# Performance work log

Measured on AMD Instinct MI355X. Metric: run time of the kernel, lower is better.

Reference implementation:

```python
import math
import jax, jax.numpy as jnp
import numpy as np

PH, PW = 16, 16
MAPPER_X = [0, 0, 6, 0, 0, 1, 1, 4, 5, 1, 3, 0, 0, 0, 3, 2]
MAPPER_Y = [0, 1, 0, 5, 2, 0, 2, 0, 0, 6, 0, 4, 6, 3, 5, 2]


def _make_dct_bases(ph, pw, mapper_x, mapper_y):
    bases = []
    for u, v in zip(mapper_x, mapper_y):
        Bu = np.cos(np.pi * (np.arange(ph) + 0.5) * u / ph) / math.sqrt(ph)
        if u != 0:
            Bu = Bu * math.sqrt(2)
        Bv = np.cos(np.pi * (np.arange(pw) + 0.5) * v / pw) / math.sqrt(pw)
        if v != 0:
            Bv = Bv * math.sqrt(2)
        bases.append(np.outer(Bu, Bv))
    return jnp.asarray(np.stack(bases, axis=0), dtype=jnp.float32)  # [M, ph, pw]


def setup_inputs() -> dict:
    key = jax.random.key(0)
    x = jax.random.normal(key, (16, 64, 224, 224), dtype=jnp.float32)
    dct_bases = _make_dct_bases(PH, PW, MAPPER_X, MAPPER_Y)
    return {"x": x, "dct_bases": dct_bases}


def reference(x, dct_bases):
    # x: [B, C, H, W]; dct_bases: [M, ph, pw]
    B, C, H, W = x.shape
    M, ph, pw = dct_bases.shape
    # H, W chosen divisible by ph, pw -> pad_h = pad_w = 0 (faithful to the no-pad path)
    Hp, Wp = H // ph, W // pw
    x_mean = x.mean(axis=1)                              # [B, H, W]
    patches = x_mean.reshape(B, Hp, ph, Wp, pw)          # non-overlapping unfold
    coeff = jnp.einsum('bhiwj,mij->bmhw', patches, dct_bases)  # [B, M, Hp, Wp]
    # nearest upsample by (ph, pw): broadcast each coeff over its patch footprint
    freq = jnp.broadcast_to(coeff[:, :, :, None, :, None], (B, M, Hp, ph, Wp, pw))
    return freq.reshape(B, M, H, W)
```

## Files before the change

### kernel.cpp

```cpp
#include <hip/hip_runtime.h>

#define B_   16
#define C_   64
#define H_   224
#define W_   224
#define M_   16
#define PH   16
#define PW   16
#define HP   14
#define WP   14
#define PLANE  (H_ * W_)
#define PLANE4 (PLANE / 4)
#define W4     (W_ / 4)
#define NSPLIT 2
#define CW     (W_ / NSPLIT)
#define CW4    (CW / 4)
#define WPB    (WP / NSPLIT)
#define SLOTS  (PH * CW4)
#define LSTW   116

typedef float f4 __attribute__((ext_vector_type(4)));

__global__ __launch_bounds__(256)
void k_fused(const float* __restrict__ x, const float* __restrict__ bases,
             float* __restrict__ out) {
    const int cb = blockIdx.x;
    const int hp = blockIdx.y;
    const int b  = blockIdx.z;
    const int t  = threadIdx.x;

    __shared__ float band[PH][LSTW];
    __shared__ float bs[M_ * PH * PW];
    __shared__ float cf[M_][WPB];

    {
        const f4* bsrc = (const f4*)bases;
        f4* bdst = (f4*)bs;
#pragma unroll
        for (int i = 0; i < 4; ++i)
            bdst[t + i * 256] = bsrc[t + i * 256];
    }

    {
        const int j0 = t;
        const int j1 = t + 256;
        const int r0 = j0 / CW4, c0 = j0 % CW4;
        const int r1 = j1 / CW4, c1 = j1 % CW4;
        const f4* p0 = (const f4*)x + (size_t)b * C_ * PLANE4
                     + (hp * PH + r0) * W4 + cb * CW4 + c0;
        const f4* p1 = (const f4*)x + (size_t)b * C_ * PLANE4
                     + (hp * PH + r1) * W4 + cb * CW4 + c1;
        f4 a0 = {0.f, 0.f, 0.f, 0.f};
        f4 a1 = {0.f, 0.f, 0.f, 0.f};
        if (j1 < SLOTS) {
#pragma unroll 8
            for (int c = 0; c < C_; ++c) {
                a0 += __builtin_nontemporal_load(&p0[(size_t)c * PLANE4]);
                a1 += __builtin_nontemporal_load(&p1[(size_t)c * PLANE4]);
            }
        } else {
#pragma unroll 8
            for (int c = 0; c < C_; ++c)
                a0 += __builtin_nontemporal_load(&p0[(size_t)c * PLANE4]);
        }
        const float inv = 1.f / (float)C_;
        a0 *= inv; a1 *= inv;
        *(f4*)&band[r0][c0 * 4] = a0;
        if (j1 < SLOTS) *(f4*)&band[r1][c1 * 4] = a1;
    }
    __syncthreads();

    if (t < M_ * WPB) {
        const int m  = t / WPB;
        const int wp = t % WPB;
        const float* bm = &bs[m * PH * PW];
        f4 sv = {0.f, 0.f, 0.f, 0.f};
#pragma unroll
        for (int r = 0; r < PH; ++r) {
#pragma unroll
            for (int q = 0; q < 4; ++q) {
                f4 bv = *(const f4*)&band[r][wp * PW + q * 4];
                f4 mv = *(const f4*)&bm[r * PW + q * 4];
                sv += bv * mv;
            }
        }
        cf[m][wp] = sv.x + sv.y + sv.z + sv.w;
    }
    __syncthreads();

    f4* dst = (f4*)out + (size_t)(b * M_) * PLANE4 + (hp * PH) * W4 + cb * CW4;
#pragma unroll
    for (int it = 0; it < (M_ * SLOTS) / 256; ++it) {
        const int idx = it * 256 + t;
        const int m   = idx / SLOTS;
        const int j   = idx % SLOTS;
        const int r   = j / CW4, c4 = j % CW4;
        const float v = cf[m][c4 >> 2];
        f4 vv = {v, v, v, v};
        __builtin_nontemporal_store(vv, &dst[(size_t)m * PLANE4 + r * W4 + c4]);
    }
}

extern "C" void kernel_launch(void* const* d_in, const int* in_sizes, int n_in,
                              void* d_out, int out_size, void* d_ws, size_t ws_size,
                              hipStream_t stream) {
    const float* x     = (const float*)d_in[0];
    const float* bases = (const float*)d_in[1];
    float* out         = (float*)d_out;

    dim3 g(NSPLIT, HP, B_);
    k_fused<<<g, 256, 0, stream>>>(x, bases, out);
}
```

Baseline: 282.6 us.

## Split width into seven blocks and channels across thread halves

After: 280.6 us. About the same (-0.7%).

```diff
diff --git a/kernel.cpp b/kernel.cpp
--- a/kernel.cpp
+++ b/kernel.cpp
@@ -12,12 +12,12 @@
 #define PLANE  (H_ * W_)
 #define PLANE4 (PLANE / 4)
 #define W4     (W_ / 4)
-#define NSPLIT 2
+#define NSPLIT 7
 #define CW     (W_ / NSPLIT)
 #define CW4    (CW / 4)
 #define WPB    (WP / NSPLIT)
 #define SLOTS  (PH * CW4)
-#define LSTW   116
+#define LSTW   36
 
 typedef float f4 __attribute__((ext_vector_type(4)));
 
@@ -29,7 +29,7 @@
     const int b  = blockIdx.z;
     const int t  = threadIdx.x;
 
-    __shared__ float band[PH][LSTW];
+    __shared__ float band2[2][PH][LSTW];
     __shared__ float bs[M_ * PH * PW];
     __shared__ float cf[M_][WPB];
 
@@ -42,59 +42,55 @@
     }
 
     {
-        const int j0 = t;
-        const int j1 = t + 256;
-        const int r0 = j0 / CW4, c0 = j0 % CW4;
-        const int r1 = j1 / CW4, c1 = j1 % CW4;
-        const f4* p0 = (const f4*)x + (size_t)b * C_ * PLANE4
-                     + (hp * PH + r0) * W4 + cb * CW4 + c0;
-        const f4* p1 = (const f4*)x + (size_t)b * C_ * PLANE4
-                     + (hp * PH + r1) * W4 + cb * CW4 + c1;
-        f4 a0 = {0.f, 0.f, 0.f, 0.f};
-        f4 a1 = {0.f, 0.f, 0.f, 0.f};
-        if (j1 < SLOTS) {
+        const int j     = t & 127;
+        const int chalf = t >> 7;
+        const int r  = j >> 3;
+        const int c4 = j & 7;
+        const f4* p = (const f4*)x + (size_t)b * C_ * PLANE4
+                    + (size_t)(chalf * 32) * PLANE4
+                    + (hp * PH + r) * W4 + cb * CW4 + c4;
+        f4 a = {0.f, 0.f, 0.f, 0.f};
 #pragma unroll 8
-            for (int c = 0; c < C_; ++c) {
-                a0 += __builtin_nontemporal_load(&p0[(size_t)c * PLANE4]);
-                a1 += __builtin_nontemporal_load(&p1[(size_t)c * PLANE4]);
-            }
-        } else {
-#pragma unroll 8
-            for (int c = 0; c < C_; ++c)
-                a0 += __builtin_nontemporal_load(&p0[(size_t)c * PLANE4]);
-        }
-        const float inv = 1.f / (float)C_;
-        a0 *= inv; a1 *= inv;
-        *(f4*)&band[r0][c0 * 4] = a0;
-        if (j1 < SLOTS) *(f4*)&band[r1][c1 * 4] = a1;
+        for (int i = 0; i < 32; ++i)
+            a += __builtin_nontemporal_load(&p[(size_t)i * PLANE4]);
+        *(f4*)&band2[chalf][r][c4 * 4] = a;
     }
     __syncthreads();
 
-    if (t < M_ * WPB) {
-        const int m  = t / WPB;
-        const int wp = t % WPB;
+    {
+        const int g   = t >> 3;
+        const int m   = g >> 1;
+        const int wpl = g & 1;
+        const int rp  = t & 7;
         const float* bm = &bs[m * PH * PW];
         f4 sv = {0.f, 0.f, 0.f, 0.f};
 #pragma unroll
-        for (int r = 0; r < PH; ++r) {
+        for (int rr = 0; rr < 2; ++rr) {
+            const int r = rp * 2 + rr;
 #pragma unroll
             for (int q = 0; q < 4; ++q) {
-                f4 bv = *(const f4*)&band[r][wp * PW + q * 4];
+                f4 bv = *(const f4*)&band2[0][r][wpl * PW + q * 4]
+                      + *(const f4*)&band2[1][r][wpl * PW + q * 4];
                 f4 mv = *(const f4*)&bm[r * PW + q * 4];
                 sv += bv * mv;
             }
         }
-        cf[m][wp] = sv.x + sv.y + sv.z + sv.w;
+        float s = sv.x + sv.y + sv.z + sv.w;
+        s += __shfl_xor(s, 1);
+        s += __shfl_xor(s, 2);
+        s += __shfl_xor(s, 4);
+        if (rp == 0) cf[m][wpl] = s * (1.f / (float)C_);
     }
     __syncthreads();
 
-    f4* dst = (f4*)out + (size_t)(b * M_) * PLANE4 + (hp * PH) * W4 + cb * CW4;
+    f4* dst = (f4*)out + (size_t)b * M_ * PLANE4 + (hp * PH) * W4 + cb * CW4;
 #pragma unroll
     for (int it = 0; it < (M_ * SLOTS) / 256; ++it) {
         const int idx = it * 256 + t;
-        const int m   = idx / SLOTS;
-        const int j   = idx % SLOTS;
-        const int r   = j / CW4, c4 = j % CW4;
+        const int m   = idx >> 7;
+        const int j   = idx & 127;
+        const int r   = j >> 3;
+        const int c4  = j & 7;
         const float v = cf[m][c4 >> 2];
         f4 vv = {v, v, v, v};
         __builtin_nontemporal_store(vv, &dst[(size_t)m * PLANE4 + r * W4 + c4]);
```
